# Optimization experiments

Measured on AMD Instinct MI355X. Metric: run time of the kernel, lower is better.

Reference implementation:

```python
import jax, jax.numpy as jnp
import numpy as np

B, N, IN_F, OUT_F = 32, 1024, 256, 256
ALPHA = 0.2  # LeakyReLU negative slope
NEG_INF = -9e15  # matches torch's -9000000000000000.0 masking constant


def setup_inputs() -> dict:
    key = jax.random.key(0)
    k1, k2, k3, k4 = jax.random.split(key, 4)
    h = jax.random.normal(k1, (B, N, IN_F), dtype=jnp.float32)
    adj = jax.random.randint(k2, (B, N, N), 0, 2, dtype=jnp.int32)
    W = jax.random.normal(k3, (OUT_F, IN_F), dtype=jnp.float32) * 0.05
    a = jax.random.normal(k4, (1, 2 * OUT_F), dtype=jnp.float32) * 0.05
    return {"h": h, "adj": adj, "W": W, "a": a}


def reference(h, adj, W, a):
    # Wh: (B, N, out)
    Wh = jnp.einsum("bni,oi->bno", h, W)
    # Decompose a([Wh_i || Wh_j]) = Wh_i . a1 + Wh_j . a2 (identical math,
    # avoids the O(B*N^2*2*out) concat intermediate of the torch code).
    a1 = a[0, :OUT_F]   # (out,)
    a2 = a[0, OUT_F:]   # (out,)
    si = Wh @ a1        # (B, N) score contribution of source node i
    sj = Wh @ a2        # (B, N) score contribution of neighbor node j
    e = jax.nn.leaky_relu(si[:, :, None] + sj[:, None, :], negative_slope=ALPHA)
    attention = jnp.where(adj > 0, e, NEG_INF)
    attention = jax.nn.softmax(attention, axis=-1)
    # dropout omitted (eval mode)
    h_prime = jnp.einsum("bij,bjo->bio", attention, Wh)
    return jax.nn.elu(h_prime)
```

## Files before the change

kernel.cpp:

```cpp
#include <hip/hip_runtime.h>
#include <hip/hip_bf16.h>


#define ALPHA 0.2f
#define LOG2E 1.44269504f

typedef __bf16 bf16x8 __attribute__((ext_vector_type(8)));
typedef __bf16 bf16x4 __attribute__((ext_vector_type(4)));
typedef float  f32x4  __attribute__((ext_vector_type(4)));
typedef unsigned long long u64;

__global__ __launch_bounds__(256) void k1_gemm1(const float* __restrict__ h,
                                                const float* __restrict__ W,
                                                const float* __restrict__ a_g,
                                                __bf16* __restrict__ whT,
                                                float* __restrict__ si,
                                                float* __restrict__ sj) {
    __shared__ __bf16 hA[64 * 72];
    __shared__ __bf16 hB[256 * 72];
    __shared__ float  red[512];
    const int t    = threadIdx.x;
    const int r0   = blockIdx.x * 64;
    const int b    = r0 >> 10;
    const int n0   = r0 & 1023;
    const int w    = t >> 6;
    const int l    = t & 63;
    const int ln   = l & 15;
    const int quad = l >> 4;

    f32x4 acc[4][4] = {};
    float4 ha_r[4], wb_r[16];

    #pragma unroll
    for (int it = 0; it < 4; ++it)
        ha_r[it] = *(const float4*)&h[(size_t)(r0 + it * 16 + (t >> 4)) * 256 + (t & 15) * 4];
    #pragma unroll
    for (int it = 0; it < 16; ++it)
        wb_r[it] = *(const float4*)&W[(size_t)(it * 16 + (t >> 4)) * 256 + (t & 15) * 4];

    for (int kc = 0; kc < 4; ++kc) {
        #pragma unroll
        for (int it = 0; it < 4; ++it) {
            const float4 v = ha_r[it];
            bf16x4 pv = {(__bf16)v.x, (__bf16)v.y, (__bf16)v.z, (__bf16)v.w};
            *(bf16x4*)&hA[(it * 16 + (t >> 4)) * 72 + (t & 15) * 4] = pv;
        }
        #pragma unroll
        for (int it = 0; it < 16; ++it) {
            const float4 v = wb_r[it];
            bf16x4 pv = {(__bf16)v.x, (__bf16)v.y, (__bf16)v.z, (__bf16)v.w};
            *(bf16x4*)&hB[(it * 16 + (t >> 4)) * 72 + (t & 15) * 4] = pv;
        }
        __syncthreads();
        if (kc < 3) {
            const int k0 = (kc + 1) * 64;
            #pragma unroll
            for (int it = 0; it < 4; ++it)
                ha_r[it] = *(const float4*)&h[(size_t)(r0 + it * 16 + (t >> 4)) * 256 + k0 + (t & 15) * 4];
            #pragma unroll
            for (int it = 0; it < 16; ++it)
                wb_r[it] = *(const float4*)&W[(size_t)(it * 16 + (t >> 4)) * 256 + k0 + (t & 15) * 4];
        }
        #pragma unroll
        for (int kk = 0; kk < 2; ++kk) {
            bf16x8 af[4], bfr[4];
            #pragma unroll
            for (int ri = 0; ri < 4; ++ri)
                af[ri] = *(const bf16x8*)&hA[(ri * 16 + ln) * 72 + kk * 32 + quad * 8];
            #pragma unroll
            for (int oi = 0; oi < 4; ++oi)
                bfr[oi] = *(const bf16x8*)&hB[(w * 64 + oi * 16 + ln) * 72 + kk * 32 + quad * 8];
            #pragma unroll
            for (int ri = 0; ri < 4; ++ri)
                #pragma unroll
                for (int oi = 0; oi < 4; ++oi)
                    acc[ri][oi] = __builtin_amdgcn_mfma_f32_16x16x32_bf16(
                        af[ri], bfr[oi], acc[ri][oi], 0, 0, 0);
        }
        __syncthreads();
    }

    #pragma unroll
    for (int ri = 0; ri < 4; ++ri) {
        const int n = ri * 16 + quad * 4;
        #pragma unroll
        for (int oi = 0; oi < 4; ++oi) {
            const int o = w * 64 + oi * 16 + ln;
            bf16x4 pv = {(__bf16)acc[ri][oi][0], (__bf16)acc[ri][oi][1],
                         (__bf16)acc[ri][oi][2], (__bf16)acc[ri][oi][3]};
            *(bf16x4*)&hB[o * 72 + n] = pv;
        }
    }
    __syncthreads();

    #pragma unroll
    for (int it = 0; it < 8; ++it) {
        const int o   = w * 64 + it * 8 + (l >> 3);
        const int seg = l & 7;
        const bf16x8 v = *(const bf16x8*)&hB[o * 72 + seg * 8];
        *(bf16x8*)&whT[((size_t)b * 256 + o) * 1024 + n0 + seg * 8] = v;
    }

    {
        float s1 = 0.f, s2 = 0.f;
        #pragma unroll 8
        for (int oi = 0; oi < 64; ++oi) {
            const int o = w * 64 + oi;
            const float v = (float)hB[o * 72 + l];
            s1 += v * a_g[o];
            s2 += v * a_g[256 + o];
        }
        red[w * 64 + l]       = s1;
        red[256 + w * 64 + l] = s2;
    }
    __syncthreads();
    if (t < 64) {
        si[b * 1024 + n0 + t] =
            (red[t] + red[64 + t] + red[128 + t] + red[192 + t]) * LOG2E;
    } else if (t < 128) {
        const int n = t - 64;
        sj[b * 1024 + n0 + n] =
            (red[256 + n] + red[320 + n] + red[384 + n] + red[448 + n]) * LOG2E;
    }
}

__global__ __launch_bounds__(256) void k3_attn(const int* __restrict__ adj,
                                               const __bf16* __restrict__ whT,
                                               const float* __restrict__ si_g,
                                               const float* __restrict__ sj_g,
                                               float* __restrict__ out) {
    __shared__ __bf16 lds_s[2][64 * 72];
    __shared__ float  lds_denom[64];
    const int t = threadIdx.x;
    const int orig = blockIdx.x;
    const int wgid = (orig & 7) * 64 + (orig >> 3);
    const int b    = wgid >> 4;
    const int i0   = (wgid & 15) << 6;
    const int w    = t >> 6;
    const int l    = t & 63;
    const int ln   = l & 15;
    const int quad = l >> 4;
    const int g    = t >> 4;
    const int j4   = t & 15;

    float si_r[4];
    #pragma unroll
    for (int m = 0; m < 4; ++m) si_r[m] = si_g[b * 1024 + i0 + m * 16 + g];

    float dsum[4] = {0.f, 0.f, 0.f, 0.f};
    f32x4 acc[4][4] = {};
    const __bf16* whTb = whT + (size_t)b * 256 * 1024;
    const int*    adjb = adj + ((size_t)(b * 1024 + i0)) * 1024;

    int4   amsk[4];
    float4 sjv;
    #pragma unroll
    for (int m = 0; m < 4; ++m)
        amsk[m] = *(const int4*)&adjb[(size_t)(m * 16 + g) * 1024 + j4 * 4];
    sjv = *(const float4*)&sj_g[b * 1024 + j4 * 4];

    #pragma unroll 2
    for (int jc = 0; jc < 16; ++jc) {
        const int j0 = jc * 64;
        __bf16* s_buf = (__bf16*)lds_s[jc & 1];

        bf16x8 bfr[2][4];
        #pragma unroll
        for (int kk = 0; kk < 2; ++kk)
            #pragma unroll
            for (int oi = 0; oi < 4; ++oi)
                bfr[kk][oi] = *(const bf16x8*)&whTb[
                    (size_t)(w * 64 + oi * 16 + ln) * 1024 + j0 + kk * 32 + quad * 8];

        #pragma unroll
        for (int m = 0; m < 4; ++m) {
            const int il = m * 16 + g;
            float e0 = si_r[m] + sjv.x; e0 = e0 > 0.f ? e0 : ALPHA * e0;
            float e1 = si_r[m] + sjv.y; e1 = e1 > 0.f ? e1 : ALPHA * e1;
            float e2 = si_r[m] + sjv.z; e2 = e2 > 0.f ? e2 : ALPHA * e2;
            float e3 = si_r[m] + sjv.w; e3 = e3 > 0.f ? e3 : ALPHA * e3;
            const float w0 = amsk[m].x > 0 ? exp2f(e0) : 0.f;
            const float w1 = amsk[m].y > 0 ? exp2f(e1) : 0.f;
            const float w2 = amsk[m].z > 0 ? exp2f(e2) : 0.f;
            const float w3 = amsk[m].w > 0 ? exp2f(e3) : 0.f;
            bf16x4 pv = {(__bf16)w0, (__bf16)w1, (__bf16)w2, (__bf16)w3};
            dsum[m] += (float)pv[0] + (float)pv[1] + (float)pv[2] + (float)pv[3];
            *(bf16x4*)&s_buf[il * 72 + j4 * 4] = pv;
        }

        if (jc < 15) {
            #pragma unroll
            for (int m = 0; m < 4; ++m)
                amsk[m] = *(const int4*)&adjb[(size_t)(m * 16 + g) * 1024 + j0 + 64 + j4 * 4];
            sjv = *(const float4*)&sj_g[b * 1024 + j0 + 64 + j4 * 4];
        }
        __syncthreads();

        #pragma unroll
        for (int kk = 0; kk < 2; ++kk) {
            bf16x8 af[4];
            #pragma unroll
            for (int ri = 0; ri < 4; ++ri)
                af[ri] = *(const bf16x8*)&s_buf[(ri * 16 + ln) * 72 + kk * 32 + quad * 8];
            #pragma unroll
            for (int ri = 0; ri < 4; ++ri)
                #pragma unroll
                for (int oi = 0; oi < 4; ++oi)
                    acc[ri][oi] = __builtin_amdgcn_mfma_f32_16x16x32_bf16(
                        af[ri], bfr[kk][oi], acc[ri][oi], 0, 0, 0);
        }
    }

    #pragma unroll
    for (int m = 0; m < 4; ++m) {
        float v = dsum[m];
        v += __shfl_xor(v, 1);
        v += __shfl_xor(v, 2);
        v += __shfl_xor(v, 4);
        v += __shfl_xor(v, 8);
        if (j4 == 0) lds_denom[m * 16 + g] = v;
    }
    __syncthreads();
    #pragma unroll
    for (int ri = 0; ri < 4; ++ri) {
        #pragma unroll
        for (int q = 0; q < 4; ++q) {
            const int il = ri * 16 + quad * 4 + q;
            const float dinv = 1.0f / fmaxf(lds_denom[il], 1e-30f);
            #pragma unroll
            for (int oi = 0; oi < 4; ++oi) {
                const int o = w * 64 + oi * 16 + ln;
                const float v = acc[ri][oi][q] * dinv;
                const float r = v > 0.f ? v : __expf(v) - 1.f;
                out[((size_t)(b * 1024 + i0 + il)) * 256 + o] = r;
            }
        }
    }
}

extern "C" void kernel_launch(void* const* d_in, const int* in_sizes, int n_in,
                              void* d_out, int out_size, void* d_ws, size_t ws_size,
                              hipStream_t stream) {
    const float* h   = (const float*)d_in[0];
    const int*   adj = (const int*)d_in[1];
    const float* W   = (const float*)d_in[2];
    const float* a   = (const float*)d_in[3];
    float* out = (float*)d_out;

    __bf16* whT = (__bf16*)d_ws;
    float*  si  = (float*)((char*)d_ws + (size_t)16777216);
    float*  sj  = (float*)((char*)d_ws + (size_t)16777216 + 131072);

    k1_gemm1<<<512, 256, 0, stream>>>(h, W, a, whT, si, sj);
    k3_attn<<<512, 256, 0, stream>>>(adj, whT, si, sj, out);
}
```

Before: 257.4 us.

## Widen attention kernel to 1024 threads with LDS-staged Wh tiles

The attention kernel now runs 16 waves per block instead of 4. Each wave computes a 64x16 output slice and each thread builds the probabilities for a single row. Wh^T tiles are prefetched into registers and staged through shared memory, so every wave reads its B fragment from LDS rather than from global memory. MFMA sections are wrapped in s_setprio. The goal is better latency hiding of adjacency loads and exp work through more resident waves, at the cost of an extra barrier per chunk, about 45KB of LDS per block, and a tight register budget from the (1024,8) launch bounds.

After: 251.5 us. 2.3% less time.

```diff
diff --git a/kernel.cpp b/kernel.cpp
--- a/kernel.cpp
+++ b/kernel.cpp
@@ -124,12 +124,13 @@
     }
 }
 
-__global__ __launch_bounds__(256) void k3_attn(const int* __restrict__ adj,
-                                               const __bf16* __restrict__ whT,
-                                               const float* __restrict__ si_g,
-                                               const float* __restrict__ sj_g,
-                                               float* __restrict__ out) {
-    __shared__ __bf16 lds_s[2][64 * 72];
+__global__ __launch_bounds__(1024, 8) void k3_attn(const int* __restrict__ adj,
+                                                   const __bf16* __restrict__ whT,
+                                                   const float* __restrict__ si_g,
+                                                   const float* __restrict__ sj_g,
+                                                   float* __restrict__ out) {
+    __shared__ __bf16 lds_w[256 * 72];
+    __shared__ __bf16 lds_s[64 * 72];
     __shared__ float  lds_denom[64];
     const int t = threadIdx.x;
     const int orig = blockIdx.x;
@@ -140,85 +141,80 @@
     const int l    = t & 63;
     const int ln   = l & 15;
     const int quad = l >> 4;
-    const int g    = t >> 4;
+    const int rowg = t >> 4;
     const int j4   = t & 15;
-
-    float si_r[4];
-    #pragma unroll
-    for (int m = 0; m < 4; ++m) si_r[m] = si_g[b * 1024 + i0 + m * 16 + g];
-
-    float dsum[4] = {0.f, 0.f, 0.f, 0.f};
-    f32x4 acc[4][4] = {};
+    const int bs   = b * 1024;
+
+    const float si0 = si_g[bs + i0 + rowg];
+
+    float dsum = 0.f;
+    f32x4 acc[4] = {};
     const __bf16* whTb = whT + (size_t)b * 256 * 1024;
-    const int*    adjb = adj + ((size_t)(b * 1024 + i0)) * 1024;
-
-    int4   amsk[4];
-    float4 sjv;
-    #pragma unroll
-    for (int m = 0; m < 4; ++m)
-        amsk[m] = *(const int4*)&adjb[(size_t)(m * 16 + g) * 1024 + j4 * 4];
-    sjv = *(const float4*)&sj_g[b * 1024 + j4 * 4];
-
-    #pragma unroll 2
+    const int*    adjb = adj + ((size_t)(bs + i0)) * 1024;
+
+    bf16x8 vreg[2];
+    int4   a_c;
+    float4 sj_c;
+
+    #pragma unroll
+    for (int it = 0; it < 2; ++it)
+        vreg[it] = *(const bf16x8*)&whTb[(size_t)(it * 128 + (t >> 3)) * 1024 + (t & 7) * 8];
+    a_c  = *(const int4*)&adjb[(size_t)rowg * 1024 + j4 * 4];
+    sj_c = *(const float4*)&sj_g[bs + j4 * 4];
+
     for (int jc = 0; jc < 16; ++jc) {
         const int j0 = jc * 64;
-        __bf16* s_buf = (__bf16*)lds_s[jc & 1];
-
-        bf16x8 bfr[2][4];
-        #pragma unroll
-        for (int kk = 0; kk < 2; ++kk)
-            #pragma unroll
-            for (int oi = 0; oi < 4; ++oi)
-                bfr[kk][oi] = *(const bf16x8*)&whTb[
-                    (size_t)(w * 64 + oi * 16 + ln) * 1024 + j0 + kk * 32 + quad * 8];
-
-        #pragma unroll
-        for (int m = 0; m < 4; ++m) {
-            const int il = m * 16 + g;
-            float e0 = si_r[m] + sjv.x; e0 = e0 > 0.f ? e0 : ALPHA * e0;
-            float e1 = si_r[m] + sjv.y; e1 = e1 > 0.f ? e1 : ALPHA * e1;
-            float e2 = si_r[m] + sjv.z; e2 = e2 > 0.f ? e2 : ALPHA * e2;
-            float e3 = si_r[m] + sjv.w; e3 = e3 > 0.f ? e3 : ALPHA * e3;
-            const float w0 = amsk[m].x > 0 ? exp2f(e0) : 0.f;
-            const float w1 = amsk[m].y > 0 ? exp2f(e1) : 0.f;
-            const float w2 = amsk[m].z > 0 ? exp2f(e2) : 0.f;
-            const float w3 = amsk[m].w > 0 ? exp2f(e3) : 0.f;
+        #pragma unroll
+        for (int it = 0; it < 2; ++it)
+            *(bf16x8*)&lds_w[(it * 128 + (t >> 3)) * 72 + (t & 7) * 8] = vreg[it];
+        if (jc < 15) {
+            #pragma unroll
+            for (int it = 0; it < 2; ++it)
+                vreg[it] = *(const bf16x8*)&whTb[
+                    (size_t)(it * 128 + (t >> 3)) * 1024 + j0 + 64 + (t & 7) * 8];
+        }
+        {
+            float e0 = si0 + sj_c.x; e0 = fmaxf(e0, ALPHA * e0);
+            float e1 = si0 + sj_c.y; e1 = fmaxf(e1, ALPHA * e1);
+            float e2 = si0 + sj_c.z; e2 = fmaxf(e2, ALPHA * e2);
+            float e3 = si0 + sj_c.w; e3 = fmaxf(e3, ALPHA * e3);
+            const float w0 = a_c.x > 0 ? exp2f(e0) : 0.f;
+            const float w1 = a_c.y > 0 ? exp2f(e1) : 0.f;
+            const float w2 = a_c.z > 0 ? exp2f(e2) : 0.f;
+            const float w3 = a_c.w > 0 ? exp2f(e3) : 0.f;
             bf16x4 pv = {(__bf16)w0, (__bf16)w1, (__bf16)w2, (__bf16)w3};
-            dsum[m] += (float)pv[0] + (float)pv[1] + (float)pv[2] + (float)pv[3];
-            *(bf16x4*)&s_buf[il * 72 + j4 * 4] = pv;
-        }
-
+            dsum += (float)pv[0] + (float)pv[1] + (float)pv[2] + (float)pv[3];
+            *(bf16x4*)&lds_s[rowg * 72 + j4 * 4] = pv;
+        }
         if (jc < 15) {
-            #pragma unroll
-            for (int m = 0; m < 4; ++m)
-                amsk[m] = *(const int4*)&adjb[(size_t)(m * 16 + g) * 1024 + j0 + 64 + j4 * 4];
-            sjv = *(const float4*)&sj_g[b * 1024 + j0 + 64 + j4 * 4];
-        }
-        __syncthreads();
-
+            a_c  = *(const int4*)&adjb[(size_t)rowg * 1024 + j0 + 64 + j4 * 4];
+            sj_c = *(const float4*)&sj_g[bs + j0 + 64 + j4 * 4];
+        }
+        __syncthreads();
+        __builtin_amdgcn_s_setprio(1);
         #pragma unroll
         for (int kk = 0; kk < 2; ++kk) {
             bf16x8 af[4];
             #pragma unroll
             for (int ri = 0; ri < 4; ++ri)
-                af[ri] = *(const bf16x8*)&s_buf[(ri * 16 + ln) * 72 + kk * 32 + quad * 8];
-            #pragma unroll
-            for (int ri = 0; ri < 4; ++ri)
-                #pragma unroll
-                for (int oi = 0; oi < 4; ++oi)
-                    acc[ri][oi] = __builtin_amdgcn_mfma_f32_16x16x32_bf16(
-                        af[ri], bfr[kk][oi], acc[ri][oi], 0, 0, 0);
-        }
-    }
-
-    #pragma unroll
-    for (int m = 0; m < 4; ++m) {
-        float v = dsum[m];
+                af[ri] = *(const bf16x8*)&lds_s[(ri * 16 + ln) * 72 + kk * 32 + quad * 8];
+            const bf16x8 bfr = *(const bf16x8*)&lds_w[(w * 16 + ln) * 72 + kk * 32 + quad * 8];
+            #pragma unroll
+            for (int ri = 0; ri < 4; ++ri)
+                acc[ri] = __builtin_amdgcn_mfma_f32_16x16x32_bf16(
+                    af[ri], bfr, acc[ri], 0, 0, 0);
+        }
+        __builtin_amdgcn_s_setprio(0);
+        __syncthreads();
+    }
+
+    {
+        float v = dsum;
         v += __shfl_xor(v, 1);
         v += __shfl_xor(v, 2);
         v += __shfl_xor(v, 4);
         v += __shfl_xor(v, 8);
-        if (j4 == 0) lds_denom[m * 16 + g] = v;
+        if (j4 == 0) lds_denom[rowg] = v;
     }
     __syncthreads();
     #pragma unroll
@@ -227,13 +223,9 @@
         for (int q = 0; q < 4; ++q) {
             const int il = ri * 16 + quad * 4 + q;
             const float dinv = 1.0f / fmaxf(lds_denom[il], 1e-30f);
-            #pragma unroll
-            for (int oi = 0; oi < 4; ++oi) {
-                const int o = w * 64 + oi * 16 + ln;
-                const float v = acc[ri][oi][q] * dinv;
-                const float r = v > 0.f ? v : __expf(v) - 1.f;
-                out[((size_t)(b * 1024 + i0 + il)) * 256 + o] = r;
-            }
+            const float v = acc[ri][q] * dinv;
+            const float r = v > 0.f ? v : __expf(v) - 1.f;
+            out[((size_t)(bs + i0 + il)) * 256 + w * 16 + ln] = r;
         }
     }
 }
@@ -252,5 +244,5 @@
     float*  sj  = (float*)((char*)d_ws + (size_t)16777216 + 131072);
 
     k1_gemm1<<<512, 256, 0, stream>>>(h, W, a, whT, si, sj);
-    k3_attn<<<512, 256, 0, stream>>>(adj, whT, si, sj, out);
+    k3_attn<<<512, 1024, 0, stream>>>(adj, whT, si, sj, out);
 }
```
